# Kernel tuning notes

Hardware: AMD Instinct MI355X
Metric: run time of the kernel (lower is better)

## Reference

```python
import jax, jax.numpy as jnp
import numpy as np

V, E, U, L, B, T = 32000, 512, 1024, 2, 32, 256


def layernorm(x, g, b, eps=1e-3):  # keras LayerNormalization default eps=1e-3
    mu = jnp.mean(x, axis=-1, keepdims=True)
    var = jnp.mean(jnp.square(x - mu), axis=-1, keepdims=True)
    return (x - mu) / jnp.sqrt(var + eps) * g + b


def masked_lstm(xs, mask, W, Uw, b, h0, c0):
    """Keras-semantics masked LSTM. xs:[B,T,D], mask:[B,T] bool.
    Masked steps: state unchanged, output = previous output (zeros before first valid step).
    Gate order i,f,g,o as in keras."""
    def step(carry, inp):
        h, c, o_prev = carry
        x_t, m = inp  # [B,D], [B]
        z = x_t @ W + h @ Uw + b  # [B,4U]
        i, f, g, o = jnp.split(z, 4, axis=-1)
        c_new = jax.nn.sigmoid(f) * c + jax.nn.sigmoid(i) * jnp.tanh(g)
        h_new = jax.nn.sigmoid(o) * jnp.tanh(c_new)
        m_ = m[:, None]
        h2 = jnp.where(m_, h_new, h)
        c2 = jnp.where(m_, c_new, c)
        out = jnp.where(m_, h_new, o_prev)
        return (h2, c2, out), out

    xs_t = jnp.swapaxes(xs, 0, 1)      # [T,B,D]
    mask_t = jnp.swapaxes(mask, 0, 1)  # [T,B]
    (h, c, _), outs = jax.lax.scan(step, (h0, c0, jnp.zeros_like(h0)), (xs_t, mask_t))
    return jnp.swapaxes(outs, 0, 1), h, c


def setup_inputs() -> dict:
    key = jax.random.key(0)
    ks = jax.random.split(key, 16)
    w = lambda k, shape, s=0.05: (jax.random.normal(k, shape) * s).astype(jnp.float32)
    inp = {}
    inp["x"] = jax.random.randint(ks[0], (B, T), 0, V)
    inp["emb"] = w(ks[1], (V, E), 0.001)
    dims = [E, U]  # layer0 takes emb, layer1 takes units
    ki = 2
    for i, d in enumerate(dims):
        for pre in ("f", "b"):
            inp[f"{pre}W{i}"] = w(ks[ki], (d, 4 * U)); ki += 1
            inp[f"{pre}U{i}"] = w(ks[ki], (U, 4 * U)); ki += 1
            inp[f"{pre}b{i}"] = jnp.zeros((4 * U,), jnp.float32)
        inp[f"g{i}"] = jnp.ones((U,), jnp.float32)
        inp[f"be{i}"] = jnp.zeros((U,), jnp.float32)
    return inp


def reference(x, emb, fW0, fU0, fb0, bW0, bU0, bb0, g0, be0,
              fW1, fU1, fb1, bW1, bU1, bb1, g1, be1):
    mask = x != 0               # mask_zero embedding mask
    e = emb[x]                  # [B,T,E]
    fxs, bxs = e[:, :-1], e[:, 1:]
    fm, bm = mask[:, :-1], mask[:, 1:]
    b_ = x.shape[0]
    fh = fc = bh = bc = jnp.zeros((b_, U), e.dtype)
    layers = [((fW0, fU0, fb0), (bW0, bU0, bb0), (g0, be0)),
              ((fW1, fU1, fb1), (bW1, bU1, bb1), (g1, be1))]
    for fp, bp, lp in layers:
        fxs, fh, fc = masked_lstm(fxs, fm, *fp, fh, fc)
        fxs = layernorm(fxs, *lp)
        # go_backwards: reverse inputs+mask, scan, LN (per-step, order-free), reverse back
        brev, bh, bc = masked_lstm(bxs[:, ::-1], bm[:, ::-1], *bp, bh, bc)
        bxs = layernorm(brev, *lp)[:, ::-1]   # NOTE: source bug uses fln for both dirs
    return fxs, bxs
```

## Files before the change

### kernel.cpp

```cpp
#include <hip/hip_runtime.h>
#include <hip/hip_bf16.h>


#define B_  32
#define T_  256
#define TS  255
#define E_  512
#define U_  1024
#define G4  4096
#define ROWS 8160
#define SROWS 8192

typedef __attribute__((ext_vector_type(8))) short short8;
typedef __attribute__((ext_vector_type(16))) float f32x16;

static __device__ __forceinline__ unsigned short f2bf(float f) {
    union { float f; unsigned int u; } x; x.f = f;
    unsigned int u = x.u;
    unsigned int r = (u + 0x7FFFu + ((u >> 16) & 1u)) >> 16;
    return (unsigned short)r;
}
static __device__ __forceinline__ float bf2f(unsigned short u) {
    union { unsigned int u; float f; } x; x.u = ((unsigned int)u) << 16;
    return x.f;
}
static __device__ __forceinline__ float sigm(float x) { return 1.f / (1.f + __expf(-x)); }
static __device__ __forceinline__ float tanh_(float x) { return 2.f / (1.f + __expf(-2.f * x)) - 1.f; }

static __device__ __forceinline__ void gload_lds16(const void* g, void* l) {
    __builtin_amdgcn_global_load_lds(
        (const __attribute__((address_space(1))) unsigned int*)g,
        (__attribute__((address_space(3))) unsigned int*)l, 16, 0, 0);
}

__global__ __launch_bounds__(256) void gather_kernel(const int* __restrict__ x,
                                                     const float* __restrict__ emb,
                                                     unsigned short* __restrict__ ebf) {
    const int bt = blockIdx.x;
    const int tok = x[bt];
    const float* src = emb + (size_t)tok * E_;
    const int c = threadIdx.x * 2;
    float2 v = *(const float2*)(src + c);
    unsigned int pk = (unsigned int)f2bf(v.x) | ((unsigned int)f2bf(v.y) << 16);
    *(unsigned int*)(ebf + (size_t)bt * E_ + c) = pk;
}

__global__ __launch_bounds__(256) void pack_frag(const float* __restrict__ src,
                                                 unsigned short* __restrict__ dst,
                                                 int KK16, int PERM) {
    const int fid = blockIdx.x * 4 + (threadIdx.x >> 6);
    const int lane = threadIdx.x & 63;
    const int tau = fid / KK16;
    const int kk = fid - tau * KK16;
    int vcol = tau * 32 + (lane & 31);
    int col;
    if (PERM) {
        int wc = vcol >> 6, g = (vcol >> 4) & 3, uu = vcol & 15;
        col = g * 1024 + wc * 16 + uu;
    } else col = vcol;
    const int k0 = kk * 16 + ((lane >> 5) << 3);
    unsigned int pk[4];
#pragma unroll
    for (int jj = 0; jj < 4; ++jj) {
        float v0 = src[(size_t)(k0 + jj * 2) * G4 + col];
        float v1 = src[(size_t)(k0 + jj * 2 + 1) * G4 + col];
        pk[jj] = (unsigned int)f2bf(v0) | ((unsigned int)f2bf(v1) << 16);
    }
    uint4 o; o.x = pk[0]; o.y = pk[1]; o.z = pk[2]; o.w = pk[3];
    *(uint4*)(dst + ((size_t)fid * 64 + lane) * 8) = o;
}

template <int KK16>
__global__ __launch_bounds__(256) void gemm_xw(
    const unsigned short* __restrict__ Abase, unsigned long long adstride,
    const unsigned short* __restrict__ P0, const unsigned short* __restrict__ P1,
    const float* __restrict__ bias0, const float* __restrict__ bias1,
    unsigned short* __restrict__ C)
{
    constexpr int K = KK16 * 16;
    constexpr int NT = KK16 / 4;
    __shared__ unsigned short alds[2][128 * 64];
    const int bm = blockIdx.x, bn = blockIdx.y, dir = blockIdx.z;
    const unsigned short* A = Abase + (size_t)dir * adstride;
    const unsigned short* P = dir ? P1 : P0;
    const float* bias = dir ? bias1 : bias0;
    unsigned short* Cd = C + (size_t)dir * SROWS * G4;
    const int tid = threadIdx.x, w = tid >> 6, lane = tid & 63;
    const int l31 = lane & 31, lhi = lane >> 5;

    f32x16 acc0, acc1;
#pragma unroll
    for (int i = 0; i < 16; ++i) { acc0[i] = 0.f; acc1[i] = 0.f; }

    const int swz_in = (lane & 7) * 16;

#define STAGE(buf, kt)                                                                     \
    {                                                                                      \
        _Pragma("unroll")                                                                  \
        for (int i = 0; i < 4; ++i) {                                                      \
            const int idx = w * 4 + i;                                                     \
            const int row = idx * 8 + (lane >> 3);                                         \
            const int inrow = swz_in ^ ((row & 7) << 4);                                   \
            const unsigned short* src = A + (size_t)(bm * 128 + row) * K + (kt) * 64 + (inrow >> 1); \
            gload_lds16(src, (char*)&alds[buf][0] + idx * 1024);                           \
        }                                                                                  \
    }

    STAGE(0, 0);
    __syncthreads();
    for (int kt = 0; kt < NT; ++kt) {
        if (kt + 1 < NT) STAGE((kt + 1) & 1, kt + 1);
        const char* ab = (const char*)&alds[kt & 1][0];
        const int arow = w * 32 + l31;
#pragma unroll
        for (int kk = 0; kk < 4; ++kk) {
            const int koff = (kk * 32 + lhi * 16) ^ ((arow & 7) << 4);
            short8 af = *(const short8*)(ab + arow * 128 + koff);
            short8 bf0 = *(const short8*)(P + ((size_t)((bn * 2 + 0) * KK16 + kt * 4 + kk) * 64 + lane) * 8);
            short8 bf1 = *(const short8*)(P + ((size_t)((bn * 2 + 1) * KK16 + kt * 4 + kk) * 64 + lane) * 8);
            acc0 = __builtin_amdgcn_mfma_f32_32x32x16_bf16(af, bf0, acc0, 0, 0, 0);
            acc1 = __builtin_amdgcn_mfma_f32_32x32x16_bf16(af, bf1, acc1, 0, 0, 0);
        }
        __syncthreads();
    }
#undef STAGE
    const int col0 = bn * 64 + l31;
    const int col1 = col0 + 32;
    const float bv0 = bias[col0], bv1 = bias[col1];
#pragma unroll
    for (int reg = 0; reg < 16; ++reg) {
        const int r = (reg & 3) + 8 * (reg >> 2) + 4 * lhi;
        const size_t row = (size_t)bm * 128 + w * 32 + r;
        Cd[row * G4 + col0] = f2bf(acc0[reg] + bv0);
        Cd[row * G4 + col1] = f2bf(acc1[reg] + bv1);
    }
}

template <int LAYER>
__global__ __launch_bounds__(512, 2) void scan_kernel(
    const unsigned short* __restrict__ puF, const unsigned short* __restrict__ puB,
    const unsigned short* __restrict__ Xw,
    const int* __restrict__ xtok,
    unsigned short* __restrict__ hcomm,
    float* __restrict__ hstate, float* __restrict__ cstate,
    unsigned short* __restrict__ out0,
    unsigned int* __restrict__ flags)
{
    constexpr int PH = (LAYER == 0) ? 0 : 1;
    __shared__ unsigned short h_lds[32768];
    __shared__ float zbuf[8][32][33];

    const int wg = blockIdx.x, dir = wg >> 5, wq = wg & 31;
    const int tid = threadIdx.x;
    const int w = tid >> 6, lane = tid & 63;
    const int ct = w & 3, kh = w >> 2;
    const int l31 = lane & 31, lhi = lane >> 5;
    const unsigned short* pu = dir ? puB : puF;

    short8 wf[32];
    {
        const int tau = wq * 4 + ct;
#pragma unroll
        for (int kkL = 0; kkL < 32; ++kkL)
            wf[kkL] = *(const short8*)(pu + (((size_t)tau * 64 + kh * 32 + kkL) * 64 + lane) * 8);
    }

    const int b = tid >> 4, up = tid & 15, uu0 = up * 2;
    const int ch = up >> 3;
    const int um = (up & 7) * 2;
    const int ucol = wq * 32 + uu0;
    const int sbase = (dir * 32 + b) * U_ + ucol;
    float c0 = cstate[sbase], c1 = cstate[sbase + 1];
    float h0 = hstate[sbase], h1 = hstate[sbase + 1];
    float o0 = 0.f, o1 = 0.f;
    const unsigned short* xwbase = Xw + (size_t)dir * SROWS * G4;

    for (int s = 0; s < TS; ++s) {
        const int tcol = dir ? (TS - s) : s;
        {
            const char* hrd = (const char*)(hcomm +
                ((size_t)((s + PH) & 1) * 2 + dir) * (32 * U_));
            uint4 hv[8];
#pragma unroll
            for (int j = 0; j < 8; ++j) {
                const void* src = hrd + ((size_t)j * 512 + tid) * 16;
                asm volatile("global_load_dwordx4 %0, %1, off sc0 sc1"
                             : "=v"(hv[j]) : "v"(src));
            }
            asm volatile("s_waitcnt vmcnt(0)" ::: "memory");
            __builtin_amdgcn_sched_barrier(0);
#pragma unroll
            for (int j = 0; j < 8; ++j) {
                const int gidx = j * 512 + tid;
                const int r = gidx >> 7;
                const int off = (gidx & 127) * 16;
                *(uint4*)((char*)h_lds + r * 2048 + (off ^ ((r & 7) << 4))) = hv[j];
            }
        }
        const size_t xr = (LAYER == 0) ? ((size_t)b * T_ + tcol) : ((size_t)s * 32 + b);
        const unsigned short* xp = xwbase + xr * G4 + ucol;
        const unsigned int xwi = *(const unsigned int*)(xp);
        const unsigned int xwf = *(const unsigned int*)(xp + 1024);
        const unsigned int xwg = *(const unsigned int*)(xp + 2048);
        const unsigned int xwo = *(const unsigned int*)(xp + 3072);
        const int m = xtok[b * T_ + tcol] != 0;
        __syncthreads();

        f32x16 acc;
#pragma unroll
        for (int i = 0; i < 16; ++i) acc[i] = 0.f;
        {
            const char* hb = (const char*)h_lds + l31 * 2048;
            const int swz = (l31 & 7) << 4;
#pragma unroll
            for (int kkL = 0; kkL < 32; ++kkL) {
                const int koff = (((kh * 32 + kkL) * 32) + lhi * 16) ^ swz;
                short8 af = *(const short8*)(hb + koff);
                acc = __builtin_amdgcn_mfma_f32_32x32x16_bf16(af, wf[kkL], acc, 0, 0, 0);
            }
        }
#pragma unroll
        for (int reg = 0; reg < 16; ++reg) {
            const int zr = (reg & 3) + 8 * (reg >> 2) + 4 * lhi;
            zbuf[w][zr][l31] = acc[reg];
        }
        __syncthreads();

        {
            float z[4][2];
#pragma unroll
            for (int g = 0; g < 4; ++g)
#pragma unroll
                for (int j = 0; j < 2; ++j) {
                    const int lv = ch * 64 + g * 16 + um + j;
                    const int ctl = lv >> 5, c32 = lv & 31;
                    z[g][j] = zbuf[ctl][b][c32] + zbuf[4 + ctl][b][c32];
                }
            z[0][0] += bf2f((unsigned short)(xwi & 0xffff)); z[0][1] += bf2f((unsigned short)(xwi >> 16));
            z[1][0] += bf2f((unsigned short)(xwf & 0xffff)); z[1][1] += bf2f((unsigned short)(xwf >> 16));
            z[2][0] += bf2f((unsigned short)(xwg & 0xffff)); z[2][1] += bf2f((unsigned short)(xwg >> 16));
            z[3][0] += bf2f((unsigned short)(xwo & 0xffff)); z[3][1] += bf2f((unsigned short)(xwo >> 16));

            float cn = sigm(z[1][0]) * c0 + sigm(z[0][0]) * tanh_(z[2][0]);
            float hn = sigm(z[3][0]) * tanh_(cn);
            if (m) { c0 = cn; h0 = hn; o0 = hn; }
            cn = sigm(z[1][1]) * c1 + sigm(z[0][1]) * tanh_(z[2][1]);
            hn = sigm(z[3][1]) * tanh_(cn);
            if (m) { c1 = cn; h1 = hn; o1 = hn; }

            unsigned short* hwr = hcomm + (size_t)((s + PH + 1) & 1) * (2 * 32 * U_);
            __hip_atomic_store((unsigned int*)(hwr + sbase),
                               (unsigned int)f2bf(h0) | ((unsigned int)f2bf(h1) << 16),
                               __ATOMIC_RELAXED, __HIP_MEMORY_SCOPE_AGENT);
            const size_t orow = (size_t)dir * SROWS + (size_t)s * 32 + b;
            *(unsigned int*)(out0 + orow * U_ + ucol) =
                (unsigned int)f2bf(o0) | ((unsigned int)f2bf(o1) << 16);
        }
        __syncthreads();

        if (tid == 0)
            __hip_atomic_store(flags + dir * 32 + wq, (unsigned int)(s + 1),
                               __ATOMIC_RELAXED, __HIP_MEMORY_SCOPE_AGENT);
        if (tid < 32) {
            while (true) {
                unsigned int v = __hip_atomic_load(flags + dir * 32 + tid,
                                                   __ATOMIC_RELAXED, __HIP_MEMORY_SCOPE_AGENT);
                if (__all((int)v > s)) break;
                __builtin_amdgcn_s_sleep(1);
            }
        }
        __syncthreads();
    }
    hstate[sbase] = h0; hstate[sbase + 1] = h1;
    cstate[sbase] = c0; cstate[sbase + 1] = c1;
}

__global__ __launch_bounds__(256) void ln_kernel(const unsigned short* __restrict__ in,
                                                 const float* __restrict__ gamma,
                                                 const float* __restrict__ beta,
                                                 unsigned short* __restrict__ outbf,
                                                 float* __restrict__ outf,
                                                 int final_) {
    const int r = blockIdx.x;
    const int dir = blockIdx.y;
    const int s = r >> 5, bb = r & 31;
    const size_t rowoff = ((size_t)dir * SROWS + r) * U_;
    const int tid = threadIdx.x;
    const int c = tid * 4;

    uint2 raw = *(const uint2*)(in + rowoff + c);
    float v0 = bf2f((unsigned short)(raw.x & 0xffff));
    float v1 = bf2f((unsigned short)(raw.x >> 16));
    float v2 = bf2f((unsigned short)(raw.y & 0xffff));
    float v3 = bf2f((unsigned short)(raw.y >> 16));

    float sum = v0 + v1 + v2 + v3;
    float sq = v0 * v0 + v1 * v1 + v2 * v2 + v3 * v3;
#pragma unroll
    for (int off = 32; off > 0; off >>= 1) {
        sum += __shfl_down(sum, off);
        sq  += __shfl_down(sq, off);
    }
    __shared__ float red[8];
    __shared__ float stats[2];
    const int wv = tid >> 6;
    if ((tid & 63) == 0) { red[wv] = sum; red[4 + wv] = sq; }
    __syncthreads();
    if (tid == 0) {
        float S = red[0] + red[1] + red[2] + red[3];
        float Q = red[4] + red[5] + red[6] + red[7];
        float mu = S * (1.f / 1024.f);
        float var = Q * (1.f / 1024.f) - mu * mu;
        stats[0] = mu;
        stats[1] = rsqrtf(var + 1e-3f);
    }
    __syncthreads();
    const float mu = stats[0], inv = stats[1];
    float y0 = (v0 - mu) * inv * gamma[c]     + beta[c];
    float y1 = (v1 - mu) * inv * gamma[c + 1] + beta[c + 1];
    float y2 = (v2 - mu) * inv * gamma[c + 2] + beta[c + 2];
    float y3 = (v3 - mu) * inv * gamma[c + 3] + beta[c + 3];

    if (!final_) {
        uint2 o;
        o.x = (unsigned int)f2bf(y0) | ((unsigned int)f2bf(y1) << 16);
        o.y = (unsigned int)f2bf(y2) | ((unsigned int)f2bf(y3) << 16);
        *(uint2*)(outbf + rowoff + c) = o;
    } else {
        const size_t tIdx = dir ? (size_t)(254 - s) : (size_t)s;
        const size_t o = (size_t)dir * ROWS * U_ + ((size_t)bb * TS + tIdx) * U_ + c;
        float4 y; y.x = y0; y.y = y1; y.z = y2; y.w = y3;
        *(float4*)(outf + o) = y;
    }
}

extern "C" void kernel_launch(void* const* d_in, const int* in_sizes, int n_in,
                              void* d_out, int out_size, void* d_ws, size_t ws_size,
                              hipStream_t stream) {
    (void)in_sizes; (void)n_in; (void)out_size; (void)ws_size;
    const int*   x   = (const int*)d_in[0];
    const float* emb = (const float*)d_in[1];
    const float* fW0 = (const float*)d_in[2];
    const float* fU0 = (const float*)d_in[3];
    const float* fb0 = (const float*)d_in[4];
    const float* bW0 = (const float*)d_in[5];
    const float* bU0 = (const float*)d_in[6];
    const float* bb0 = (const float*)d_in[7];
    const float* g0  = (const float*)d_in[8];
    const float* be0 = (const float*)d_in[9];
    const float* fW1 = (const float*)d_in[10];
    const float* fU1 = (const float*)d_in[11];
    const float* fb1 = (const float*)d_in[12];
    const float* bW1 = (const float*)d_in[13];
    const float* bU1 = (const float*)d_in[14];
    const float* bb1 = (const float*)d_in[15];
    const float* g1  = (const float*)d_in[16];
    const float* be1 = (const float*)d_in[17];

    const size_t MB8  = 8388608;
    const size_t MB4  = 4194304;
    char* ws = (char*)d_ws;
    char* S0 = ws;
    unsigned short* ebf  = (unsigned short*)(S0);
    unsigned short* pu0f = (unsigned short*)(S0 + MB8);
    unsigned short* pu0b = (unsigned short*)(S0 + 2 * MB8);
    unsigned short* pw0f = (unsigned short*)(S0 + 3 * MB8);
    unsigned short* pw0b = (unsigned short*)(S0 + 3 * MB8 + MB4);
    unsigned short* x1   = (unsigned short*)(S0);
    char* S1 = ws + 4 * MB8;
    unsigned short* pw1f = (unsigned short*)(S1);
    unsigned short* pw1b = (unsigned short*)(S1 + MB8);
    unsigned short* pu1f = (unsigned short*)(S1);
    unsigned short* pu1b = (unsigned short*)(S1 + MB8);
    unsigned short* out0 = (unsigned short*)(ws + 6 * MB8);
    unsigned short* Xw   = (unsigned short*)(ws + 10 * MB8);
    char* stateblob = ws + 26 * MB8;
    unsigned short* hcomm = (unsigned short*)stateblob;
    float* hstate = (float*)(stateblob + 262144);
    float* cstate = (float*)(stateblob + 524288);
    unsigned int* flags = (unsigned int*)(stateblob + 786432);

    hipMemsetAsync(stateblob, 0, 786432 + 1024, stream);

    gather_kernel<<<dim3(B_ * T_), 256, 0, stream>>>(x, emb, ebf);

    pack_frag<<<dim3(128 * 64 / 4), 256, 0, stream>>>(fU0, pu0f, 64, 1);
    pack_frag<<<dim3(128 * 64 / 4), 256, 0, stream>>>(bU0, pu0b, 64, 1);
    pack_frag<<<dim3(128 * 32 / 4), 256, 0, stream>>>(fW0, pw0f, 32, 0);
    pack_frag<<<dim3(128 * 32 / 4), 256, 0, stream>>>(bW0, pw0b, 32, 0);
    pack_frag<<<dim3(128 * 64 / 4), 256, 0, stream>>>(fW1, pw1f, 64, 0);
    pack_frag<<<dim3(128 * 64 / 4), 256, 0, stream>>>(bW1, pw1b, 64, 0);

    gemm_xw<32><<<dim3(64, 64, 2), 256, 0, stream>>>(ebf, 0ull, pw0f, pw0b, fb0, bb0, Xw);
    scan_kernel<0><<<dim3(64), 512, 0, stream>>>(pu0f, pu0b, Xw, x, hcomm, hstate, cstate, out0, flags);
    ln_kernel<<<dim3(ROWS, 2), 256, 0, stream>>>(out0, g0, be0, x1, nullptr, 0);
    gemm_xw<64><<<dim3(64, 64, 2), 256, 0, stream>>>(x1, (unsigned long long)SROWS * U_, pw1f, pw1b, fb1, bb1, Xw);
    pack_frag<<<dim3(128 * 64 / 4), 256, 0, stream>>>(fU1, pu1f, 64, 1);
    pack_frag<<<dim3(128 * 64 / 4), 256, 0, stream>>>(bU1, pu1b, 64, 1);
    scan_kernel<1><<<dim3(64), 512, 0, stream>>>(pu1f, pu1b, Xw, x, hcomm, hstate, cstate, out0, flags + 64);
    ln_kernel<<<dim3(ROWS, 2), 256, 0, stream>>>(out0, g1, be1, nullptr, (float*)d_out, 1);
}
```

Before: 2.490 ms.

## Replace flag barrier with step-tagged hidden-state exchange in LSTM scan

The per-step cross-workgroup flag barrier is removed. Each hidden value is now stored as a 32-bit word pairing the bf16 value with a 16-bit step tag, and readers spin on the state buffer until every tag matches the expected step. This takes the separate flag store, the polling loop and an extra block barrier off the serial critical path. In exchange, the communicated state doubles in size and the whole block re-reads the buffer on any mismatch. The old scan_kernel is left behind with dead leftover code and is no longer launched.

```diff
diff --git a/kernel.cpp b/kernel.cpp
--- a/kernel.cpp
+++ b/kernel.cpp
@@ -141,12 +141,11 @@
     const unsigned short* __restrict__ puF, const unsigned short* __restrict__ puB,
     const unsigned short* __restrict__ Xw,
     const int* __restrict__ xtok,
-    unsigned short* __restrict__ hcomm,
-    float* __restrict__ hstate, float* __restrict__ cstate,
-    unsigned short* __restrict__ out0,
-    unsigned int* __restrict__ flags)
+    unsigned int* __restrict__ hcommT,
+    float* __restrict__ hstate, float* __restrict__ cstate)
 {
-    constexpr int PH = (LAYER == 0) ? 0 : 1;
+    constexpr int PH   = (LAYER == 0) ? 0 : 1;
+    constexpr int BASE = (LAYER == 0) ? 0 : 255;
     __shared__ unsigned short h_lds[32768];
     __shared__ float zbuf[8][32][33];
 
@@ -174,29 +173,11 @@
     float h0 = hstate[sbase], h1 = hstate[sbase + 1];
     float o0 = 0.f, o1 = 0.f;
     const unsigned short* xwbase = Xw + (size_t)dir * SROWS * G4;
+    unsigned short* out0 = (unsigned short*)0;
+    (void)out0;
 
     for (int s = 0; s < TS; ++s) {
         const int tcol = dir ? (TS - s) : s;
-        {
-            const char* hrd = (const char*)(hcomm +
-                ((size_t)((s + PH) & 1) * 2 + dir) * (32 * U_));
-            uint4 hv[8];
-#pragma unroll
-            for (int j = 0; j < 8; ++j) {
-                const void* src = hrd + ((size_t)j * 512 + tid) * 16;
-                asm volatile("global_load_dwordx4 %0, %1, off sc0 sc1"
-                             : "=v"(hv[j]) : "v"(src));
-            }
-            asm volatile("s_waitcnt vmcnt(0)" ::: "memory");
-            __builtin_amdgcn_sched_barrier(0);
-#pragma unroll
-            for (int j = 0; j < 8; ++j) {
-                const int gidx = j * 512 + tid;
-                const int r = gidx >> 7;
-                const int off = (gidx & 127) * 16;
-                *(uint4*)((char*)h_lds + r * 2048 + (off ^ ((r & 7) << 4))) = hv[j];
-            }
-        }
         const size_t xr = (LAYER == 0) ? ((size_t)b * T_ + tcol) : ((size_t)s * 32 + b);
         const unsigned short* xp = xwbase + xr * G4 + ucol;
         const unsigned int xwi = *(const unsigned int*)(xp);
@@ -204,7 +185,43 @@
         const unsigned int xwg = *(const unsigned int*)(xp + 2048);
         const unsigned int xwo = *(const unsigned int*)(xp + 3072);
         const int m = xtok[b * T_ + tcol] != 0;
-        __syncthreads();
+
+        {
+            const unsigned int exp_ = (unsigned int)(BASE + s) & 0xFFFFu;
+            const unsigned int* hrd = hcommT +
+                ((size_t)((s + PH) & 1) * 2 + dir) * (32 * 1024);
+            while (true) {
+                uint4 hv[16];
+#pragma unroll
+                for (int j = 0; j < 8; ++j) {
+                    const int gidx = j * 512 + tid;
+                    const unsigned int* src = hrd + (size_t)(gidx >> 7) * 1024 + (gidx & 127) * 8;
+                    asm volatile("global_load_dwordx4 %0, %1, off sc0 sc1"
+                                 : "=v"(hv[2 * j]) : "v"(src));
+                    asm volatile("global_load_dwordx4 %0, %1, off sc0 sc1"
+                                 : "=v"(hv[2 * j + 1]) : "v"(src + 4));
+                }
+                asm volatile("s_waitcnt vmcnt(0)" ::: "memory");
+                __builtin_amdgcn_sched_barrier(0);
+                unsigned int bad = 0;
+#pragma unroll
+                for (int j = 0; j < 8; ++j) {
+                    uint4 a = hv[2 * j], b2 = hv[2 * j + 1];
+                    bad |= (a.x ^ exp_) | (a.y ^ exp_) | (a.z ^ exp_) | (a.w ^ exp_)
+                         | (b2.x ^ exp_) | (b2.y ^ exp_) | (b2.z ^ exp_) | (b2.w ^ exp_);
+                    uint4 o;
+                    o.x = (a.x >> 16)  | (a.y & 0xFFFF0000u);
+                    o.y = (a.z >> 16)  | (a.w & 0xFFFF0000u);
+                    o.z = (b2.x >> 16) | (b2.y & 0xFFFF0000u);
+                    o.w = (b2.z >> 16) | (b2.w & 0xFFFF0000u);
+                    const int gidx = j * 512 + tid;
+                    const int r = gidx >> 7;
+                    const int off = (gidx & 127) * 16;
+                    *(uint4*)((char*)h_lds + r * 2048 + (off ^ ((r & 7) << 4))) = o;
+                }
+                if (!__syncthreads_or((int)(bad & 0xFFFFu))) break;
+            }
+        }
 
         f32x16 acc;
 #pragma unroll
@@ -248,28 +265,32 @@
             hn = sigm(z[3][1]) * tanh_(cn);
             if (m) { c1 = cn; h1 = hn; o1 = hn; }
 
-            unsigned short* hwr = hcomm + (size_t)((s + PH + 1) & 1) * (2 * 32 * U_);
-            __hip_atomic_store((unsigned int*)(hwr + sbase),
-                               (unsigned int)f2bf(h0) | ((unsigned int)f2bf(h1) << 16),
-                               __ATOMIC_RELAXED, __HIP_MEMORY_SCOPE_AGENT);
-            const size_t orow = (size_t)dir * SROWS + (size_t)s * 32 + b;
-            *(unsigned int*)(out0 + orow * U_ + ucol) =
-                (unsigned int)f2bf(o0) | ((unsigned int)f2bf(o1) << 16);
-        }
-        __syncthreads();
-
-        if (tid == 0)
-            __hip_atomic_store(flags + dir * 32 + wq, (unsigned int)(s + 1),
-                               __ATOMIC_RELAXED, __HIP_MEMORY_SCOPE_AGENT);
-        if (tid < 32) {
-            while (true) {
-                unsigned int v = __hip_atomic_load(flags + dir * 32 + tid,
-                                                   __ATOMIC_RELAXED, __HIP_MEMORY_SCOPE_AGENT);
-                if (__all((int)v > s)) break;
-                __builtin_amdgcn_s_sleep(1);
-            }
-        }
-        __syncthreads();
+            const unsigned int wtag = (unsigned int)(BASE + s + 1) & 0xFFFFu;
+            unsigned int* hwr = hcommT +
+                ((size_t)((s + PH + 1) & 1) * 2 + dir) * (32 * 1024) + (b * 1024 + ucol);
+            uint2 hv2;
+            hv2.x = ((unsigned int)f2bf(h0) << 16) | wtag;
+            hv2.y = ((unsigned int)f2bf(h1) << 16) | wtag;
+            asm volatile("global_store_dwordx2 %0, %1, off sc0 sc1"
+                         :: "v"(hwr), "v"(hv2) : "memory");
+        }
+        {
+            extern __shared__ char _dummy[];
+            (void)_dummy;
+        }
+        {
+        }
+        {
+        }
+        {
+        }
+        out0_write:
+        {
+        }
+        goto after_out0;
+        after_out0:
+        {
+        }
     }
     hstate[sbase] = h0; hstate[sbase + 1] = h1;
     cstate[sbase] = c0; cstate[sbase + 1] = c1;
@@ -332,6 +353,153 @@
         float4 y; y.x = y0; y.y = y1; y.z = y2; y.w = y3;
         *(float4*)(outf + o) = y;
     }
+}
+
+
+template <int LAYER>
+__global__ __launch_bounds__(512, 2) void scan_kernel2(
+    const unsigned short* __restrict__ puF, const unsigned short* __restrict__ puB,
+    const unsigned short* __restrict__ Xw,
+    const int* __restrict__ xtok,
+    unsigned int* __restrict__ hcommT,
+    float* __restrict__ hstate, float* __restrict__ cstate,
+    unsigned short* __restrict__ out0)
+{
+    constexpr int PH   = (LAYER == 0) ? 0 : 1;
+    constexpr int BASE = (LAYER == 0) ? 0 : 255;
+    __shared__ unsigned short h_lds[32768];
+    __shared__ float zbuf[8][32][33];
+
+    const int wg = blockIdx.x, dir = wg >> 5, wq = wg & 31;
+    const int tid = threadIdx.x;
+    const int w = tid >> 6, lane = tid & 63;
+    const int ct = w & 3, kh = w >> 2;
+    const int l31 = lane & 31, lhi = lane >> 5;
+    const unsigned short* pu = dir ? puB : puF;
+
+    short8 wf[32];
+    {
+        const int tau = wq * 4 + ct;
+#pragma unroll
+        for (int kkL = 0; kkL < 32; ++kkL)
+            wf[kkL] = *(const short8*)(pu + (((size_t)tau * 64 + kh * 32 + kkL) * 64 + lane) * 8);
+    }
+
+    const int b = tid >> 4, up = tid & 15, uu0 = up * 2;
+    const int ch = up >> 3;
+    const int um = (up & 7) * 2;
+    const int ucol = wq * 32 + uu0;
+    const int sbase = (dir * 32 + b) * U_ + ucol;
+    float c0 = cstate[sbase], c1 = cstate[sbase + 1];
+    float h0 = hstate[sbase], h1 = hstate[sbase + 1];
+    float o0 = 0.f, o1 = 0.f;
+    const unsigned short* xwbase = Xw + (size_t)dir * SROWS * G4;
+
+    for (int s = 0; s < TS; ++s) {
+        const int tcol = dir ? (TS - s) : s;
+        const size_t xr = (LAYER == 0) ? ((size_t)b * T_ + tcol) : ((size_t)s * 32 + b);
+        const unsigned short* xp = xwbase + xr * G4 + ucol;
+        const unsigned int xwi = *(const unsigned int*)(xp);
+        const unsigned int xwf = *(const unsigned int*)(xp + 1024);
+        const unsigned int xwg = *(const unsigned int*)(xp + 2048);
+        const unsigned int xwo = *(const unsigned int*)(xp + 3072);
+        const int m = xtok[b * T_ + tcol] != 0;
+
+        {
+            const unsigned int exp_ = (unsigned int)(BASE + s) & 0xFFFFu;
+            const unsigned int* hrd = hcommT +
+                ((size_t)((s + PH) & 1) * 2 + dir) * (32 * 1024);
+            while (true) {
+                uint4 hv[16];
+#pragma unroll
+                for (int j = 0; j < 8; ++j) {
+                    const int gidx = j * 512 + tid;
+                    const unsigned int* src = hrd + (size_t)(gidx >> 7) * 1024 + (gidx & 127) * 8;
+                    asm volatile("global_load_dwordx4 %0, %1, off sc0 sc1"
+                                 : "=v"(hv[2 * j]) : "v"(src));
+                    asm volatile("global_load_dwordx4 %0, %1, off sc0 sc1"
+                                 : "=v"(hv[2 * j + 1]) : "v"(src + 4));
+                }
+                asm volatile("s_waitcnt vmcnt(0)" ::: "memory");
+                __builtin_amdgcn_sched_barrier(0);
+                unsigned int bad = 0;
+#pragma unroll
+                for (int j = 0; j < 8; ++j) {
+                    uint4 a = hv[2 * j], b2 = hv[2 * j + 1];
+                    bad |= (a.x ^ exp_) | (a.y ^ exp_) | (a.z ^ exp_) | (a.w ^ exp_)
+                         | (b2.x ^ exp_) | (b2.y ^ exp_) | (b2.z ^ exp_) | (b2.w ^ exp_);
+                    uint4 o;
+                    o.x = (a.x >> 16)  | (a.y & 0xFFFF0000u);
+                    o.y = (a.z >> 16)  | (a.w & 0xFFFF0000u);
+                    o.z = (b2.x >> 16) | (b2.y & 0xFFFF0000u);
+                    o.w = (b2.z >> 16) | (b2.w & 0xFFFF0000u);
+                    const int gidx = j * 512 + tid;
+                    const int r = gidx >> 7;
+                    const int off = (gidx & 127) * 16;
+                    *(uint4*)((char*)h_lds + r * 2048 + (off ^ ((r & 7) << 4))) = o;
+                }
+                if (!__syncthreads_or((int)(bad & 0xFFFFu))) break;
+            }
+        }
+
+        f32x16 acc;
+#pragma unroll
+        for (int i = 0; i < 16; ++i) acc[i] = 0.f;
+        {
+            const char* hb = (const char*)h_lds + l31 * 2048;
+            const int swz = (l31 & 7) << 4;
+#pragma unroll
+            for (int kkL = 0; kkL < 32; ++kkL) {
+                const int koff = (((kh * 32 + kkL) * 32) + lhi * 16) ^ swz;
+                short8 af = *(const short8*)(hb + koff);
+                acc = __builtin_amdgcn_mfma_f32_32x32x16_bf16(af, wf[kkL], acc, 0, 0, 0);
+            }
+        }
+#pragma unroll
+        for (int reg = 0; reg < 16; ++reg) {
+            const int zr = (reg & 3) + 8 * (reg >> 2) + 4 * lhi;
+            zbuf[w][zr][l31] = acc[reg];
+        }
+        __syncthreads();
+
+        {
+            float z[4][2];
+#pragma unroll
+            for (int g = 0; g < 4; ++g)
+#pragma unroll
+                for (int j = 0; j < 2; ++j) {
+                    const int lv = ch * 64 + g * 16 + um + j;
+                    const int ctl = lv >> 5, c32 = lv & 31;
+                    z[g][j] = zbuf[ctl][b][c32] + zbuf[4 + ctl][b][c32];
+                }
+            z[0][0] += bf2f((unsigned short)(xwi & 0xffff)); z[0][1] += bf2f((unsigned short)(xwi >> 16));
+            z[1][0] += bf2f((unsigned short)(xwf & 0xffff)); z[1][1] += bf2f((unsigned short)(xwf >> 16));
+            z[2][0] += bf2f((unsigned short)(xwg & 0xffff)); z[2][1] += bf2f((unsigned short)(xwg >> 16));
+            z[3][0] += bf2f((unsigned short)(xwo & 0xffff)); z[3][1] += bf2f((unsigned short)(xwo >> 16));
+
+            float cn = sigm(z[1][0]) * c0 + sigm(z[0][0]) * tanh_(z[2][0]);
+            float hn = sigm(z[3][0]) * tanh_(cn);
+            if (m) { c0 = cn; h0 = hn; o0 = hn; }
+            cn = sigm(z[1][1]) * c1 + sigm(z[0][1]) * tanh_(z[2][1]);
+            hn = sigm(z[3][1]) * tanh_(cn);
+            if (m) { c1 = cn; h1 = hn; o1 = hn; }
+
+            const unsigned int wtag = (unsigned int)(BASE + s + 1) & 0xFFFFu;
+            unsigned int* hwr = hcommT +
+                ((size_t)((s + PH + 1) & 1) * 2 + dir) * (32 * 1024) + (b * 1024 + ucol);
+            uint2 hv2;
+            hv2.x = ((unsigned int)f2bf(h0) << 16) | wtag;
+            hv2.y = ((unsigned int)f2bf(h1) << 16) | wtag;
+            asm volatile("global_store_dwordx2 %0, %1, off sc0 sc1"
+                         :: "v"(hwr), "v"(hv2) : "memory");
+
+            const size_t orow = (size_t)dir * SROWS + (size_t)s * 32 + b;
+            *(unsigned int*)(out0 + orow * U_ + ucol) =
+                (unsigned int)f2bf(o0) | ((unsigned int)f2bf(o1) << 16);
+        }
+    }
+    hstate[sbase] = h0; hstate[sbase + 1] = h1;
+    cstate[sbase] = c0; cstate[sbase + 1] = c1;
 }
 
 extern "C" void kernel_launch(void* const* d_in, const int* in_sizes, int n_in,
@@ -357,30 +525,29 @@
     const float* g1  = (const float*)d_in[16];
     const float* be1 = (const float*)d_in[17];
 
+    const size_t MB   = 1048576;
     const size_t MB8  = 8388608;
     const size_t MB4  = 4194304;
     char* ws = (char*)d_ws;
-    char* S0 = ws;
+    unsigned int* hcommT = (unsigned int*)ws;
+    float* hstate = (float*)(ws + 512 * 1024);
+    float* cstate = (float*)(ws + 768 * 1024);
+    char* S0 = ws + 2 * MB;
     unsigned short* ebf  = (unsigned short*)(S0);
     unsigned short* pu0f = (unsigned short*)(S0 + MB8);
     unsigned short* pu0b = (unsigned short*)(S0 + 2 * MB8);
     unsigned short* pw0f = (unsigned short*)(S0 + 3 * MB8);
     unsigned short* pw0b = (unsigned short*)(S0 + 3 * MB8 + MB4);
     unsigned short* x1   = (unsigned short*)(S0);
-    char* S1 = ws + 4 * MB8;
+    char* S1 = ws + 34 * MB;
     unsigned short* pw1f = (unsigned short*)(S1);
     unsigned short* pw1b = (unsigned short*)(S1 + MB8);
     unsigned short* pu1f = (unsigned short*)(S1);
     unsigned short* pu1b = (unsigned short*)(S1 + MB8);
-    unsigned short* out0 = (unsigned short*)(ws + 6 * MB8);
-    unsigned short* Xw   = (unsigned short*)(ws + 10 * MB8);
-    char* stateblob = ws + 26 * MB8;
-    unsigned short* hcomm = (unsigned short*)stateblob;
-    float* hstate = (float*)(stateblob + 262144);
-    float* cstate = (float*)(stateblob + 524288);
-    unsigned int* flags = (unsigned int*)(stateblob + 786432);
-
-    hipMemsetAsync(stateblob, 0, 786432 + 1024, stream);
+    unsigned short* out0 = (unsigned short*)(ws + 50 * MB);
+    unsigned short* Xw   = (unsigned short*)(ws + 82 * MB);
+
+    hipMemsetAsync(ws, 0, 2 * MB, stream);
 
     gather_kernel<<<dim3(B_ * T_), 256, 0, stream>>>(x, emb, ebf);
 
@@ -392,11 +559,11 @@
     pack_frag<<<dim3(128 * 64 / 4), 256, 0, stream>>>(bW1, pw1b, 64, 0);
 
     gemm_xw<32><<<dim3(64, 64, 2), 256, 0, stream>>>(ebf, 0ull, pw0f, pw0b, fb0, bb0, Xw);
-    scan_kernel<0><<<dim3(64), 512, 0, stream>>>(pu0f, pu0b, Xw, x, hcomm, hstate, cstate, out0, flags);
+    scan_kernel2<0><<<dim3(64), 512, 0, stream>>>(pu0f, pu0b, Xw, x, hcommT, hstate, cstate, out0);
     ln_kernel<<<dim3(ROWS, 2), 256, 0, stream>>>(out0, g0, be0, x1, nullptr, 0);
     gemm_xw<64><<<dim3(64, 64, 2), 256, 0, stream>>>(x1, (unsigned long long)SROWS * U_, pw1f, pw1b, fb1, bb1, Xw);
     pack_frag<<<dim3(128 * 64 / 4), 256, 0, stream>>>(fU1, pu1f, 64, 1);
     pack_frag<<<dim3(128 * 64 / 4), 256, 0, stream>>>(bU1, pu1b, 64, 1);
-    scan_kernel<1><<<dim3(64), 512, 0, stream>>>(pu1f, pu1b, Xw, x, hcomm, hstate, cstate, out0, flags + 64);
+    scan_kernel2<1><<<dim3(64), 512, 0, stream>>>(pu1f, pu1b, Xw, x, hcommT, hstate, cstate, out0);
     ln_kernel<<<dim3(ROWS, 2), 256, 0, stream>>>(out0, g1, be1, nullptr, (float*)d_out, 1);
 }
```

Result: slower. 5.469 ms (+119.6%).
